# Performance work log

Hardware: AMD Instinct MI355X
Metric: run time of the kernel (lower is better)

Reference implementation:

```python
import jax, jax.numpy as jnp
import numpy as np
import math

B, T, D, H, K = 4, 2048, 1024, 16, 64

def setup_inputs() -> dict:
    key = jax.random.key(0)
    ks = jax.random.split(key, 6)
    scale = 1.0 / math.sqrt(D)  # keep logits in a sane range (torch code uses raw randn params)
    X = jax.random.normal(ks[0], (B, T, D), dtype=jnp.float32)
    Wq = jax.random.normal(ks[1], (H, D, K), dtype=jnp.float32) * scale
    Wk = jax.random.normal(ks[2], (H, D, K), dtype=jnp.float32) * scale
    Wv = jax.random.normal(ks[3], (H, D, K), dtype=jnp.float32) * scale
    Wo = jax.random.normal(ks[4], (H * K, H * K), dtype=jnp.float32) * (1.0 / math.sqrt(H * K))
    bo = jnp.zeros((H * K,), dtype=jnp.float32)
    return {"X": X, "Wq": Wq, "Wk": Wk, "Wv": Wv, "Wo": Wo, "bo": bo}

def reference(X, Wq, Wk, Wv, Wo, bo):
    # per-head projections: [B,H,T,K]
    q = jnp.einsum('btc,nck->bntk', X, Wq)
    k = jnp.einsum('btc,nck->bntk', X, Wk)
    v = jnp.einsum('btc,nck->bntk', X, Wv)
    # full score matrix [B,H,T,T] with causal mask (query t attends to s <= t)
    scores = jnp.einsum('bntk,bnsk->bnts', q, k) / math.sqrt(K)
    causal = jnp.tril(jnp.ones((T, T), dtype=bool))
    scores = jnp.where(causal[None, None], scores, jnp.finfo(scores.dtype).min)
    attn = jax.nn.softmax(scores, axis=-1)
    out = jnp.einsum('bnts,bnsk->bntk', attn, v)  # [B,H,T,K]
    # concat heads along feature dim (head-major ordering, matches torch.cat over heads)
    out = jnp.transpose(out, (0, 2, 1, 3)).reshape(B, T, H * K)
    # output projection (torch nn.Linear: x @ W.T + b)
    return out @ Wo.T + bo
```

## Files before the change

kernel.cpp:

```cpp
#include <hip/hip_runtime.h>
#include <hip/hip_bf16.h>
#include <math.h>

#define B_SZ 4
#define T_SZ 2048
#define D_SZ 1024
#define H_SZ 16
#define K_SZ 64

typedef __attribute__((ext_vector_type(8))) short bf8_t;
typedef __attribute__((ext_vector_type(4))) float f4_t;

__device__ __forceinline__ ushort f2bf(float f) {
    union { float f; unsigned u; } v; v.f = f;
    return (ushort)((v.u + 0x7fffu + ((v.u >> 16) & 1u)) >> 16);
}

__device__ __forceinline__ uint cvt_pk_bf16(float lo, float hi) {
    uint r;
    asm("v_cvt_pk_bf16_f32 %0, %1, %2" : "=v"(r) : "v"(lo), "v"(hi));
    return r;
}

__device__ __forceinline__ void gld_lds16(const ushort* g, ushort* l) {
    __builtin_amdgcn_global_load_lds(
        (const __attribute__((address_space(1))) void*)g,
        (__attribute__((address_space(3))) void*)l, 16, 0, 0);
}

#define Q_PRESCALE 0.18033688011112042f

__global__ __launch_bounds__(256) void convert_bf16_kernel(
    const float* __restrict__ src, ushort* __restrict__ dst)
{
    const size_t i = ((size_t)blockIdx.x * 256 + threadIdx.x) * 8;
    float4 a = *(const float4*)(src + i);
    float4 b = *(const float4*)(src + i + 4);
    ushort o[8] = {f2bf(a.x), f2bf(a.y), f2bf(a.z), f2bf(a.w),
                   f2bf(b.x), f2bf(b.y), f2bf(b.z), f2bf(b.w)};
    *(uint4*)(dst + i) = *(const uint4*)o;
}

__global__ __launch_bounds__(256) void transpose_w_kernel(
    const float* __restrict__ Wq, const float* __restrict__ Wk,
    const float* __restrict__ Wv, ushort* __restrict__ WT)
{
    __shared__ __align__(16) float tile[64][68];
    const int tid = threadIdx.x;
    const int d0  = blockIdx.x * 64;
    const int g   = blockIdx.y;
    const int sel = g >> 4, h = g & 15;
    const float* W = (sel == 0 ? Wq : (sel == 1 ? Wk : Wv)) + (size_t)h * D_SZ * K_SZ;

    {
        const int r = tid >> 2, ks = (tid & 3) * 16;
        const float4* src = (const float4*)(W + (size_t)(d0 + r) * 64 + ks);
        float4* dst = (float4*)&tile[r][ks];
        dst[0] = src[0]; dst[1] = src[1]; dst[2] = src[2]; dst[3] = src[3];
    }
    __syncthreads();
    {
        const int k = tid >> 2, ds = (tid & 3) * 16;
        ushort o[16];
        #pragma unroll
        for (int i = 0; i < 16; ++i) o[i] = f2bf(tile[ds + i][k]);
        uint4* dst = (uint4*)&WT[(size_t)(sel * 1024 + h * 64 + k) * 1024 + d0 + ds];
        dst[0] = ((const uint4*)o)[0];
        dst[1] = ((const uint4*)o)[1];
    }
}

__device__ __forceinline__ void gemm_bt_tile(
    const ushort* __restrict__ A, const ushort* __restrict__ Bt,
    int Kdim, int m0, int n0, ushort* As, ushort* Bs, f4_t acc[4][4])
{
    const int tid  = threadIdx.x;
    const int lane = tid & 63, wv = tid >> 6;
    const int l16  = lane & 15, quad = lane >> 4;
    const int wm   = (wv >> 1) * 64, wn = (wv & 1) * 64;
    const int sw   = (l16 >> 1) & 3;

    const int ra0 = tid >> 2,         qa0 = (tid & 3) ^ ((ra0 >> 1) & 3);
    const int ra1 = (tid + 256) >> 2, qa1 = (tid & 3) ^ ((ra1 >> 1) & 3);
    ushort* ldsA0 = As + (size_t)(wv * 64) * 8;
    ushort* ldsA1 = As + (size_t)(wv * 64 + 256) * 8;
    ushort* ldsB0 = Bs + (size_t)(wv * 64) * 8;
    ushort* ldsB1 = Bs + (size_t)(wv * 64 + 256) * 8;
    const ushort* gA0 = A  + (size_t)(m0 + ra0) * Kdim + qa0 * 8;
    const ushort* gA1 = A  + (size_t)(m0 + ra1) * Kdim + qa1 * 8;
    const ushort* gB0 = Bt + (size_t)(n0 + ra0) * Kdim + qa0 * 8;
    const ushort* gB1 = Bt + (size_t)(n0 + ra1) * Kdim + qa1 * 8;

    for (int k0 = 0; k0 < Kdim; k0 += 32) {
        __syncthreads();
        gld_lds16(gA0 + k0, ldsA0);
        gld_lds16(gA1 + k0, ldsA1);
        gld_lds16(gB0 + k0, ldsB0);
        gld_lds16(gB1 + k0, ldsB1);
        __syncthreads();

        bf8_t a[4], b[4];
        #pragma unroll
        for (int mt = 0; mt < 4; ++mt)
            a[mt] = *(const bf8_t*)&As[(wm + mt * 16 + l16) * 32 + ((quad ^ sw) * 8)];
        #pragma unroll
        for (int nt = 0; nt < 4; ++nt)
            b[nt] = *(const bf8_t*)&Bs[(wn + nt * 16 + l16) * 32 + ((quad ^ sw) * 8)];
        #pragma unroll
        for (int mt = 0; mt < 4; ++mt)
            #pragma unroll
            for (int nt = 0; nt < 4; ++nt)
                acc[mt][nt] = __builtin_amdgcn_mfma_f32_16x16x32_bf16(
                    a[mt], b[nt], acc[mt][nt], 0, 0, 0);
    }
}

__global__ __launch_bounds__(256) void gemm_qkv_kernel(
    const ushort* __restrict__ Xb, const ushort* __restrict__ WT,
    ushort* __restrict__ Qo, ushort* __restrict__ Ko, ushort* __restrict__ Vo)
{
    __shared__ __align__(16) ushort As[128 * 32];
    __shared__ __align__(16) ushort Bs[128 * 32];
    const int n0 = blockIdx.x * 128, m0 = blockIdx.y * 128;

    f4_t acc[4][4];
    #pragma unroll
    for (int i = 0; i < 4; ++i)
        #pragma unroll
        for (int j = 0; j < 4; ++j) acc[i][j] = (f4_t){0.f, 0.f, 0.f, 0.f};

    gemm_bt_tile(Xb, WT, 1024, m0, n0, As, Bs, acc);

    const int tid = threadIdx.x;
    const int lane = tid & 63, wv = tid >> 6;
    const int l16 = lane & 15, quad = lane >> 4;
    const int wm = (wv >> 1) * 64, wn = (wv & 1) * 64;
    const int sel = n0 >> 10;
    ushort* Out = (sel == 0 ? Qo : (sel == 1 ? Ko : Vo));
    const float osc = (sel == 0) ? Q_PRESCALE : 1.0f;

    #pragma unroll
    for (int nt = 0; nt < 4; ++nt) {
        const int col = n0 + wn + nt * 16 + l16;
        const int h = (col >> 6) & 15, kk = col & 63;
        #pragma unroll
        for (int mt = 0; mt < 4; ++mt) {
            #pragma unroll
            for (int r = 0; r < 4; ++r) {
                const int row = m0 + wm + mt * 16 + quad * 4 + r;
                const int bb = row >> 11, t = row & 2047;
                Out[((size_t)(bb * 16 + h) * 2048 + t) * 64 + kk] =
                    f2bf(acc[mt][nt][r] * osc);
            }
        }
    }
}

__global__ __launch_bounds__(256) void gemm_out_kernel(
    const ushort* __restrict__ Yb, const ushort* __restrict__ WoB,
    const float* __restrict__ bo, float* __restrict__ Out)
{
    __shared__ __align__(16) ushort As[128 * 32];
    __shared__ __align__(16) ushort Bs[128 * 32];
    const int n0 = blockIdx.x * 128, m0 = blockIdx.y * 128;

    f4_t acc[4][4];
    #pragma unroll
    for (int i = 0; i < 4; ++i)
        #pragma unroll
        for (int j = 0; j < 4; ++j) acc[i][j] = (f4_t){0.f, 0.f, 0.f, 0.f};

    gemm_bt_tile(Yb, WoB, 1024, m0, n0, As, Bs, acc);

    const int tid = threadIdx.x;
    const int lane = tid & 63, wv = tid >> 6;
    const int l16 = lane & 15, quad = lane >> 4;
    const int wm = (wv >> 1) * 64, wn = (wv & 1) * 64;

    #pragma unroll
    for (int nt = 0; nt < 4; ++nt) {
        const int col = n0 + wn + nt * 16 + l16;
        const float bias = bo[col];
        #pragma unroll
        for (int mt = 0; mt < 4; ++mt) {
            #pragma unroll
            for (int r = 0; r < 4; ++r) {
                const int row = m0 + wm + mt * 16 + quad * 4 + r;
                Out[(size_t)row * 1024 + col] = acc[mt][nt][r] + bias;
            }
        }
    }
}

__global__ __launch_bounds__(256) void transpose_v_kernel(
    const ushort* __restrict__ V, ushort* __restrict__ Vt)
{
    __shared__ __align__(16) ushort tile[64 * 74];
    const int tid = threadIdx.x;
    const int t0  = blockIdx.x * 64;
    const int bh  = blockIdx.y;

    {
        const int t = tid >> 2, ks = (tid & 3) * 16;
        const ushort* src = V + ((size_t)bh * T_SZ + t0 + t) * K_SZ + ks;
        uint4 a = *(const uint4*)src;
        uint4 b = *(const uint4*)(src + 8);
        uint* dst = (uint*)&tile[t * 74 + ks];
        dst[0] = a.x; dst[1] = a.y; dst[2] = a.z; dst[3] = a.w;
        dst[4] = b.x; dst[5] = b.y; dst[6] = b.z; dst[7] = b.w;
    }
    __syncthreads();
    {
        const int l = tid & 63, w = tid >> 6;
        #pragma unroll
        for (int kk = 0; kk < 16; ++kk) {
            const int k = w * 16 + kk;
            Vt[((size_t)bh * K_SZ + k) * T_SZ + t0 + l] = tile[l * 74 + k];
        }
    }
}

__global__ __launch_bounds__(256) void attn_mfma_kernel(
    const ushort* __restrict__ Qg, const ushort* __restrict__ Kg,
    const ushort* __restrict__ Vtg, ushort* __restrict__ Y)
{
    __shared__ __align__(16) ushort Ks[2][64 * 64];
    __shared__ __align__(16) ushort Vs[2][64 * 64];
    __shared__ __align__(16) ushort Pl[4][32 * 72];

    const int tid  = threadIdx.x;
    const int w    = tid >> 6;
    const int lane = tid & 63;
    const int l16  = lane & 15;
    const int quad = lane >> 4;
    const int qlo = blockIdx.x;
    const int qhi = 15 - qlo;
    const int bh = blockIdx.y;
    const int bb = bh >> 4, h = bh & 15;

    const int trowL = qlo * 128 + w * 32;
    const int trowH = qhi * 128 + w * 32;

    bf8_t qaL[2][2], qaH[2][2];
    #pragma unroll
    for (int mt = 0; mt < 2; ++mt) {
        const ushort* qpL = Qg + ((size_t)bh * T_SZ + trowL + mt * 16 + l16) * K_SZ + quad * 8;
        const ushort* qpH = Qg + ((size_t)bh * T_SZ + trowH + mt * 16 + l16) * K_SZ + quad * 8;
        qaL[mt][0] = *(const bf8_t*)qpL;
        qaL[mt][1] = *(const bf8_t*)(qpL + 32);
        qaH[mt][0] = *(const bf8_t*)qpH;
        qaH[mt][1] = *(const bf8_t*)(qpH + 32);
    }

    f4_t OL[2][4], OH[2][4];
    float lpL[2] = {0.f, 0.f}, lpH[2] = {0.f, 0.f};
    #pragma unroll
    for (int mt = 0; mt < 2; ++mt)
        #pragma unroll
        for (int dt = 0; dt < 4; ++dt) {
            OL[mt][dt] = (f4_t){0.f, 0.f, 0.f, 0.f};
            OH[mt][dt] = (f4_t){0.f, 0.f, 0.f, 0.f};
        }

    ushort* myP = Pl[w];
    const int g_ln = (lane & 7) ^ (lane >> 3);
    const int rr_ln = lane >> 3;

    const ushort* Kbh = Kg  + (size_t)bh * T_SZ * K_SZ;
    const ushort* Vbh = Vtg + (size_t)bh * K_SZ * T_SZ;

    const int n_it = 2 * qhi + 2;

    bf8_t kb[4][2], vb[4][2];
    int s0 = 0;
    auto tile_compute = [&](const bf8_t (&qa)[2][2], f4_t (&O)[2][4],
                            float (&lp)[2], int trow) {
        f4_t S[4][2];
        #pragma unroll
        for (int nt = 0; nt < 4; ++nt)
            #pragma unroll
            for (int mt = 0; mt < 2; ++mt) S[nt][mt] = (f4_t){0.f, 0.f, 0.f, 0.f};
        #pragma unroll
        for (int nt = 0; nt < 4; ++nt)
            #pragma unroll
            for (int mt = 0; mt < 2; ++mt) {
                S[nt][mt] = __builtin_amdgcn_mfma_f32_16x16x32_bf16(
                    kb[nt][0], qa[mt][0], S[nt][mt], 0, 0, 0);
                S[nt][mt] = __builtin_amdgcn_mfma_f32_16x16x32_bf16(
                    kb[nt][1], qa[mt][1], S[nt][mt], 0, 0, 0);
            }

        const bool diag = (s0 + 64 > trow);

        #pragma unroll
        for (int mt = 0; mt < 2; ++mt) {
            const int qg = trow + mt * 16 + l16;
            #pragma unroll
            for (int nt = 0; nt < 4; ++nt) {
                float p[4];
                if (diag) {
                    #pragma unroll
                    for (int r = 0; r < 4; ++r) {
                        float x = S[nt][mt][r];
                        if (s0 + nt * 16 + quad * 4 + r > qg) x = -1e30f;
                        p[r] = __builtin_amdgcn_exp2f(x);
                    }
                } else {
                    #pragma unroll
                    for (int r = 0; r < 4; ++r)
                        p[r] = __builtin_amdgcn_exp2f(S[nt][mt][r]);
                }
                lp[mt] += (p[0] + p[1]) + (p[2] + p[3]);
                uint2 pk;
                pk.x = cvt_pk_bf16(p[0], p[1]);
                pk.y = cvt_pk_bf16(p[2], p[3]);
                *(uint2*)&myP[(mt * 16 + l16) * 72 + nt * 16 + quad * 4] = pk;
            }
        }
        asm volatile("" ::: "memory");
        bf8_t pa[2][2];
        #pragma unroll
        for (int mt = 0; mt < 2; ++mt) {
            const ushort* pr = &myP[(mt * 16 + l16) * 72];
            pa[mt][0] = *(const bf8_t*)(pr + quad * 8);
            pa[mt][1] = *(const bf8_t*)(pr + 32 + quad * 8);
        }
        asm volatile("" ::: "memory");

        #pragma unroll
        for (int dt = 0; dt < 4; ++dt)
            #pragma unroll
            for (int mt = 0; mt < 2; ++mt) {
                O[mt][dt] = __builtin_amdgcn_mfma_f32_16x16x32_bf16(
                    pa[mt][0], vb[dt][0], O[mt][dt], 0, 0, 0);
                O[mt][dt] = __builtin_amdgcn_mfma_f32_16x16x32_bf16(
                    pa[mt][1], vb[dt][1], O[mt][dt], 0, 0, 0);
            }
    };

    #pragma unroll
    for (int j = 0; j < 2; ++j) {
        const int r8 = (j * 4 + w) * 8 + rr_ln;
        gld_lds16(Kbh + (size_t)r8 * K_SZ + g_ln * 8, &Ks[0][(j * 4 + w) * 512]);
        gld_lds16(Vbh + (size_t)r8 * T_SZ + g_ln * 8, &Vs[0][(j * 4 + w) * 512]);
    }

    int cur = 0;
    for (int it = 0; it < n_it; ++it) {
        s0 = it * 64;

        __syncthreads();
        if (it + 1 < n_it) {
            const int sn = s0 + 64, nb = cur ^ 1;
            #pragma unroll
            for (int j = 0; j < 2; ++j) {
                const int r8 = (j * 4 + w) * 8 + rr_ln;
                gld_lds16(Kbh + (size_t)(sn + r8) * K_SZ + g_ln * 8,
                          &Ks[nb][(j * 4 + w) * 512]);
                gld_lds16(Vbh + (size_t)r8 * T_SZ + sn + g_ln * 8,
                          &Vs[nb][(j * 4 + w) * 512]);
            }
        }

        const bool doH = (s0 < trowH + 32);
        const bool doL = (s0 < trowL + 32);
        if (doH || doL) {
            const ushort* Kc = Ks[cur];
            const ushort* Vc = Vs[cur];
            #pragma unroll
            for (int nt = 0; nt < 4; ++nt) {
                const int sr = nt * 16 + l16;
                kb[nt][0] = *(const bf8_t*)&Kc[sr * 64 + ((quad ^ (sr & 7)) * 8)];
                kb[nt][1] = *(const bf8_t*)&Kc[sr * 64 + (((quad + 4) ^ (sr & 7)) * 8)];
                vb[nt][0] = *(const bf8_t*)&Vc[sr * 64 + ((quad ^ (sr & 7)) * 8)];
                vb[nt][1] = *(const bf8_t*)&Vc[sr * 64 + (((quad + 4) ^ (sr & 7)) * 8)];
            }
            if (doH) tile_compute(qaH, OH, lpH, trowH);
            if (doL) tile_compute(qaL, OL, lpL, trowL);
        }
        cur ^= 1;
    }

    auto epilogue = [&](f4_t (&O)[2][4], float (&lp)[2], int trow) {
        #pragma unroll
        for (int mt = 0; mt < 2; ++mt) {
            float s = lp[mt];
            s += __shfl_xor(s, 16);
            s += __shfl_xor(s, 32);
            const float inv = 1.f / s;
            float invr[4];
            #pragma unroll
            for (int r = 0; r < 4; ++r)
                invr[r] = __shfl(inv, quad * 4 + r);
            #pragma unroll
            for (int dt = 0; dt < 4; ++dt) {
                const int col = h * 64 + dt * 16 + l16;
                #pragma unroll
                for (int r = 0; r < 4; ++r) {
                    const int tg = trow + mt * 16 + quad * 4 + r;
                    Y[((size_t)(bb * T_SZ + tg)) * (H_SZ * K_SZ) + col] =
                        f2bf(O[mt][dt][r] * invr[r]);
                }
            }
        }
    };
    epilogue(OH, lpH, trowH);
    epilogue(OL, lpL, trowL);
}

extern "C" void kernel_launch(void* const* d_in, const int* in_sizes, int n_in,
                              void* d_out, int out_size, void* d_ws, size_t ws_size,
                              hipStream_t stream) {
    const float* X  = (const float*)d_in[0];
    const float* Wq = (const float*)d_in[1];
    const float* Wk = (const float*)d_in[2];
    const float* Wv = (const float*)d_in[3];
    const float* Wo = (const float*)d_in[4];
    const float* bo = (const float*)d_in[5];
    float* out = (float*)d_out;

    const size_t NE = (size_t)B_SZ * H_SZ * T_SZ * K_SZ;
    ushort* Qb   = (ushort*)d_ws;
    ushort* Kb   = Qb + NE;
    ushort* Vb   = Kb + NE;
    ushort* Vtb  = Vb + NE;
    ushort* Yb   = Vtb + NE;
    ushort* Xb   = Yb + NE;
    ushort* WT   = Xb + NE;
    ushort* WoB  = WT + (size_t)3072 * 1024;

    convert_bf16_kernel<<<dim3(4096), 256, 0, stream>>>(X, Xb);
    convert_bf16_kernel<<<dim3(512), 256, 0, stream>>>(Wo, WoB);
    transpose_w_kernel<<<dim3(16, 48), 256, 0, stream>>>(Wq, Wk, Wv, WT);
    gemm_qkv_kernel<<<dim3(24, 64), 256, 0, stream>>>(Xb, WT, Qb, Kb, Vb);
    transpose_v_kernel<<<dim3(32, 64), 256, 0, stream>>>(Vb, Vtb);
    attn_mfma_kernel<<<dim3(8, 64), 256, 0, stream>>>(Qb, Kb, Vtb, Yb);
    gemm_out_kernel<<<dim3(8, 64), 256, 0, stream>>>(Yb, WoB, bo, out);
}
```

Measured before the change: 302.8 us.

## Restructure attention into single-wave blocks loading K/V directly to registers

```diff
diff --git a/kernel.cpp b/kernel.cpp
--- a/kernel.cpp
+++ b/kernel.cpp
@@ -220,26 +220,28 @@
     }
 }
 
-__global__ __launch_bounds__(256) void attn_mfma_kernel(
+__global__ __launch_bounds__(64, 2) void attn_mfma_kernel(
     const ushort* __restrict__ Qg, const ushort* __restrict__ Kg,
     const ushort* __restrict__ Vtg, ushort* __restrict__ Y)
 {
-    __shared__ __align__(16) ushort Ks[2][64 * 64];
-    __shared__ __align__(16) ushort Vs[2][64 * 64];
-    __shared__ __align__(16) ushort Pl[4][32 * 72];
-
-    const int tid  = threadIdx.x;
-    const int w    = tid >> 6;
-    const int lane = tid & 63;
+    __shared__ __align__(16) ushort Ph[2][32 * 72];
+
+    const int lane = threadIdx.x;
     const int l16  = lane & 15;
     const int quad = lane >> 4;
-    const int qlo = blockIdx.x;
-    const int qhi = 15 - qlo;
-    const int bh = blockIdx.y;
-    const int bb = bh >> 4, h = bh & 15;
-
-    const int trowL = qlo * 128 + w * 32;
-    const int trowH = qhi * 128 + w * 32;
+
+    const int lin = blockIdx.x;
+    const int xcd = lin & 7;
+    const int idx = lin >> 3;
+    const int bh  = xcd * 8 + (idx & 7);
+    const int jp  = idx >> 3;
+    const int bb  = bh >> 4, h = bh & 15;
+
+    const int trowL = jp * 32;
+    const int trowH = (63 - jp) * 32;
+
+    const ushort* Kbh = Kg  + (size_t)bh * T_SZ * K_SZ;
+    const ushort* Vbh = Vtg + (size_t)bh * K_SZ * T_SZ;
 
     bf8_t qaL[2][2], qaH[2][2];
     #pragma unroll
@@ -262,34 +264,32 @@
             OH[mt][dt] = (f4_t){0.f, 0.f, 0.f, 0.f};
         }
 
-    ushort* myP = Pl[w];
-    const int g_ln = (lane & 7) ^ (lane >> 3);
-    const int rr_ln = lane >> 3;
-
-    const ushort* Kbh = Kg  + (size_t)bh * T_SZ * K_SZ;
-    const ushort* Vbh = Vtg + (size_t)bh * K_SZ * T_SZ;
-
-    const int n_it = 2 * qhi + 2;
+    const int n_it = (trowH + 32 + 63) >> 6;
 
     bf8_t kb[4][2], vb[4][2];
-    int s0 = 0;
-    auto tile_compute = [&](const bf8_t (&qa)[2][2], f4_t (&O)[2][4],
-                            float (&lp)[2], int trow) {
-        f4_t S[4][2];
+    #pragma unroll
+    for (int nt = 0; nt < 4; ++nt)
+        #pragma unroll
+        for (int hh = 0; hh < 2; ++hh) {
+            kb[nt][hh] = *(const bf8_t*)&Kbh[(size_t)(nt * 16 + l16) * K_SZ + hh * 32 + quad * 8];
+            vb[nt][hh] = *(const bf8_t*)&Vbh[(size_t)(nt * 16 + l16) * T_SZ + hh * 32 + quad * 8];
+        }
+
+    auto qk = [&](const bf8_t (&qa)[2][2], f4_t (&S)[4][2]) {
         #pragma unroll
         for (int nt = 0; nt < 4; ++nt)
             #pragma unroll
-            for (int mt = 0; mt < 2; ++mt) S[nt][mt] = (f4_t){0.f, 0.f, 0.f, 0.f};
-        #pragma unroll
-        for (int nt = 0; nt < 4; ++nt)
-            #pragma unroll
             for (int mt = 0; mt < 2; ++mt) {
+                S[nt][mt] = (f4_t){0.f, 0.f, 0.f, 0.f};
                 S[nt][mt] = __builtin_amdgcn_mfma_f32_16x16x32_bf16(
                     kb[nt][0], qa[mt][0], S[nt][mt], 0, 0, 0);
                 S[nt][mt] = __builtin_amdgcn_mfma_f32_16x16x32_bf16(
                     kb[nt][1], qa[mt][1], S[nt][mt], 0, 0, 0);
             }
-
+    };
+
+    auto sm_pv = [&](f4_t (&S)[4][2], f4_t (&O)[2][4], float (&lp)[2],
+                     int trow, ushort* myP, int s0) {
         const bool diag = (s0 + 64 > trow);
 
         #pragma unroll
@@ -338,47 +338,38 @@
             }
     };
 
-    #pragma unroll
-    for (int j = 0; j < 2; ++j) {
-        const int r8 = (j * 4 + w) * 8 + rr_ln;
-        gld_lds16(Kbh + (size_t)r8 * K_SZ + g_ln * 8, &Ks[0][(j * 4 + w) * 512]);
-        gld_lds16(Vbh + (size_t)r8 * T_SZ + g_ln * 8, &Vs[0][(j * 4 + w) * 512]);
-    }
-
-    int cur = 0;
     for (int it = 0; it < n_it; ++it) {
-        s0 = it * 64;
-
-        __syncthreads();
-        if (it + 1 < n_it) {
-            const int sn = s0 + 64, nb = cur ^ 1;
-            #pragma unroll
-            for (int j = 0; j < 2; ++j) {
-                const int r8 = (j * 4 + w) * 8 + rr_ln;
-                gld_lds16(Kbh + (size_t)(sn + r8) * K_SZ + g_ln * 8,
-                          &Ks[nb][(j * 4 + w) * 512]);
-                gld_lds16(Vbh + (size_t)r8 * T_SZ + sn + g_ln * 8,
-                          &Vs[nb][(j * 4 + w) * 512]);
-            }
-        }
-
-        const bool doH = (s0 < trowH + 32);
-        const bool doL = (s0 < trowL + 32);
-        if (doH || doL) {
-            const ushort* Kc = Ks[cur];
-            const ushort* Vc = Vs[cur];
-            #pragma unroll
-            for (int nt = 0; nt < 4; ++nt) {
-                const int sr = nt * 16 + l16;
-                kb[nt][0] = *(const bf8_t*)&Kc[sr * 64 + ((quad ^ (sr & 7)) * 8)];
-                kb[nt][1] = *(const bf8_t*)&Kc[sr * 64 + (((quad + 4) ^ (sr & 7)) * 8)];
-                vb[nt][0] = *(const bf8_t*)&Vc[sr * 64 + ((quad ^ (sr & 7)) * 8)];
-                vb[nt][1] = *(const bf8_t*)&Vc[sr * 64 + (((quad + 4) ^ (sr & 7)) * 8)];
-            }
-            if (doH) tile_compute(qaH, OH, lpH, trowH);
-            if (doL) tile_compute(qaL, OL, lpL, trowL);
-        }
-        cur ^= 1;
+        const int s0 = it * 64;
+        const bool doL  = (s0 < trowL + 32);
+        const bool more = (it + 1 < n_it);
+        const int  sn   = s0 + 64;
+
+        f4_t S[4][2];
+
+        qk(qaH, S);
+        sm_pv(S, OH, lpH, trowH, Ph[0], s0);
+
+        if (doL) qk(qaL, S);
+
+        if (more) {
+            #pragma unroll
+            for (int nt = 0; nt < 4; ++nt)
+                #pragma unroll
+                for (int hh = 0; hh < 2; ++hh)
+                    kb[nt][hh] = *(const bf8_t*)&Kbh[
+                        (size_t)(sn + nt * 16 + l16) * K_SZ + hh * 32 + quad * 8];
+        }
+
+        if (doL) sm_pv(S, OL, lpL, trowL, Ph[1], s0);
+
+        if (more) {
+            #pragma unroll
+            for (int nt = 0; nt < 4; ++nt)
+                #pragma unroll
+                for (int hh = 0; hh < 2; ++hh)
+                    vb[nt][hh] = *(const bf8_t*)&Vbh[
+                        (size_t)(nt * 16 + l16) * T_SZ + sn + hh * 32 + quad * 8];
+        }
     }
 
     auto epilogue = [&](f4_t (&O)[2][4], float (&lp)[2], int trow) {
@@ -434,6 +425,6 @@
     transpose_w_kernel<<<dim3(16, 48), 256, 0, stream>>>(Wq, Wk, Wv, WT);
     gemm_qkv_kernel<<<dim3(24, 64), 256, 0, stream>>>(Xb, WT, Qb, Kb, Vb);
     transpose_v_kernel<<<dim3(32, 64), 256, 0, stream>>>(Vb, Vtb);
-    attn_mfma_kernel<<<dim3(8, 64), 256, 0, stream>>>(Qb, Kb, Vtb, Yb);
+    attn_mfma_kernel<<<dim3(2048), 64, 0, stream>>>(Qb, Kb, Vtb, Yb);
     gemm_out_kernel<<<dim3(8, 64), 256, 0, stream>>>(Yb, WoB, bo, out);
 }
```

Result: no change. 297.6 us (-1.7%).
